# Kernel optimization log

Hardware: AMD Instinct MI355X
Metric: run time of the kernel (lower is better)

## Reference

```python
import jax, jax.numpy as jnp
import numpy as np

S, HID = 2048, 4096
H, KV, D = 32, 8, 128
EPS = 1e-6
THETA = 10000.0


def setup_inputs() -> dict:
    key = jax.random.key(0)
    k0, k1, k2 = jax.random.split(key, 3)
    return {
        "positions": jnp.arange(S, dtype=jnp.int32),
        "hidden_states": jax.random.normal(k0, (S, HID), jnp.float32),
        "w_qkv": jax.random.normal(k1, ((H + 2 * KV) * D, HID), jnp.float32) * 0.02,
        "w_o": jax.random.normal(k2, (HID, H * D), jnp.float32) * 0.02,
        "gq": jnp.ones((D,), jnp.float32),
        "gk": jnp.ones((D,), jnp.float32),
    }


def _rmsnorm(x, g):
    # per-head RMSNorm over last dim (head_dim)
    return x * jax.lax.rsqrt(jnp.mean(x * x, axis=-1, keepdims=True) + EPS) * g


def _rope(x, positions):
    # NeoX-style rotary embedding, rotary_dim == head_dim
    half = D // 2
    inv_freq = 1.0 / (THETA ** (jnp.arange(half, dtype=jnp.float32) * 2.0 / D))
    freqs = positions.astype(jnp.float32)[:, None] * inv_freq  # [S, half]
    cos = jnp.cos(freqs)[:, None, :]  # [S, 1, half]
    sin = jnp.sin(freqs)[:, None, :]
    x1, x2 = x[..., :half], x[..., half:]
    return jnp.concatenate([x1 * cos - x2 * sin, x2 * cos + x1 * sin], axis=-1)


def reference(positions, hidden_states, w_qkv, w_o, gq, gk):
    qkv = hidden_states @ w_qkv.T  # [S, (H+2KV)*D]
    q = qkv[:, : H * D].reshape(S, H, D)
    k = qkv[:, H * D : (H + KV) * D].reshape(S, KV, D)
    v = qkv[:, (H + KV) * D :].reshape(S, KV, D)

    q = _rmsnorm(q, gq)
    k = _rmsnorm(k, gk)
    q = _rope(q, positions)
    k = _rope(k, positions)

    rep = H // KV
    kf = jnp.repeat(k, rep, axis=1)  # [S, H, D]
    vf = jnp.repeat(v, rep, axis=1)

    scale = D ** -0.5
    scores = jnp.einsum("qhd,khd->hqk", q, kf) * scale  # [H, S, S]
    causal = jnp.tril(jnp.ones((S, S), dtype=bool))
    scores = jnp.where(causal[None], scores, jnp.finfo(scores.dtype).min)
    attn = jax.nn.softmax(scores, axis=-1)
    ctx = jnp.einsum("hqk,khd->qhd", attn, vf).reshape(S, H * D)
    return ctx @ w_o.T  # [S, HID]
```

## Files before the change

### kernel.cpp

```cpp
#include <hip/hip_runtime.h>
#include <hip/hip_bf16.h>

#define S_LEN 2048
#define HID   4096
#define NH    32
#define NKV   8
#define DH    128
#define NQKV  ((NH + 2*NKV) * DH)

typedef __attribute__((ext_vector_type(8))) short s16x8;
typedef __attribute__((ext_vector_type(4))) short s16x4;
typedef __attribute__((ext_vector_type(4))) float f32x4;

__device__ __forceinline__ short f2bf(float x) {
    union { __hip_bfloat16 b; short s; } u;
    u.b = __float2bfloat16(x);
    return u.s;
}
__device__ __forceinline__ float bf2f(short s) {
    union { unsigned int u; float f; } v;
    v.u = ((unsigned int)(unsigned short)s) << 16;
    return v.f;
}

__device__ __forceinline__ void gload16(const void* g, void* l) {
    __builtin_amdgcn_global_load_lds(
        (const __attribute__((address_space(1))) void*)g,
        (__attribute__((address_space(3))) void*)l,
        16, 0, 0);
}

__device__ __forceinline__ void cstore(float* p, float v) { *p = v; }
__device__ __forceinline__ void cstore(short* p, float v) { *p = f2bf(v); }

__global__ __launch_bounds__(256) void convert_hs_wqkv(
        const float* __restrict__ in1, short* __restrict__ o1, long n1,
        const float* __restrict__ in2, short* __restrict__ o2, long n2)
{
    const long total = n1 + n2;
    long i0 = ((long)blockIdx.x * blockDim.x + threadIdx.x) * 4;
    long stride = (long)gridDim.x * blockDim.x * 4;
    for (long i = i0; i < total; i += stride) {
        const float* src; short* dst; long off;
        if (i < n1) { src = in1; dst = o1; off = i; }
        else        { src = in2; dst = o2; off = i - n1; }
        float4 v = *(const float4*)(src + off);
        s16x4 o;
        o[0] = f2bf(v.x); o[1] = f2bf(v.y); o[2] = f2bf(v.z); o[3] = f2bf(v.w);
        *(s16x4*)(dst + off) = o;
    }
}

template <typename OT>
__global__ __launch_bounds__(512, 2) void gemm192(
        const short* __restrict__ A, const short* __restrict__ B,
        OT* __restrict__ C, int M, int N, int K)
{
    __shared__ char lds[114688];
    const int t = threadIdx.x;
    const int w = t >> 6, l = t & 63, g = l >> 4, q16 = l & 15;
    const int wm = w >> 2, wn = w & 3;
    const int bx = blockIdx.x, by = blockIdx.y;
    const int NT = K >> 6;

    const int r0 = t >> 3, c0 = t & 7;
    const int scA = c0 ^ (r0 & 7);
    const long KB64  = (long)K * 128;
    const long KB128 = (long)K * 256;
    const long gA00 = ((long)(by * 256 + r0) * K) * 2 + scA * 16;
    long gBoff[3];
#pragma unroll
    for (int i = 0; i < 3; ++i) {
        int row = (i * 512 + t) >> 3;
        int chunk = (t & 7) ^ (row & 7);
        gBoff[i] = ((long)(bx * 192 + row) * K) * 2 + chunk * 16;
    }
    const int dstw = w * 1024;

    auto SA = [&](int kt, int h) {
        char* d = lds + ((kt & 1) * 2 + h) * 16384 + dstw;
        const long s0 = gA00 + h * KB128 + (long)kt * 128;
        gload16((const char*)A + s0, d);
        gload16((const char*)A + s0 + KB64, d + 8192);
    };
    auto SB = [&](int kt) {
        char* d = lds + 65536 + (kt & 1) * 24576 + dstw;
        const long kb = (long)kt * 128;
#pragma unroll
        for (int i = 0; i < 3; ++i)
            gload16((const char*)B + gBoff[i] + kb, d + i * 8192);
    };

    const int arow = q16 * 128;
    const int brow = (wn * 48 + q16) * 128;
    const int sw0 = ((g) ^ (q16 & 7)) << 4;
    const int sw1 = ((4 + g) ^ (q16 & 7)) << 4;

    f32x4 acc[8][3] = {};
    s16x8 a0f[4][2], a1f[4][2], bfE[3][2], bfO[3][2];

    SB(0); SA(0, 0); SA(0, 1);
    SB(1); SA(1, 0); SA(1, 1);
    asm volatile("s_waitcnt vmcnt(7)" ::: "memory");
    __builtin_amdgcn_s_barrier();
    asm volatile("" ::: "memory");
    {
        const char* As_ = lds + wm * 16384;
        const char* Bs_ = lds + 65536;
#pragma unroll
        for (int mi = 0; mi < 4; ++mi) {
            a0f[mi][0] = *(const s16x8*)(As_ + arow + mi*2048 + sw0);
            a0f[mi][1] = *(const s16x8*)(As_ + arow + mi*2048 + sw1);
        }
#pragma unroll
        for (int ni = 0; ni < 3; ++ni) {
            bfE[ni][0] = *(const s16x8*)(Bs_ + brow + ni*2048 + sw0);
            bfE[ni][1] = *(const s16x8*)(Bs_ + brow + ni*2048 + sw1);
        }
    }

#define GBODY(KT, BCUR, BNXT, PAR) do {                                       \
    const char* As_ = lds + ((PAR)*2 + wm) * 16384;                           \
                                  \
    _Pragma("unroll")                                                         \
    for (int mi = 0; mi < 4; ++mi) {                                          \
        a1f[mi][0] = *(const s16x8*)(As_ + arow + 8192 + mi*2048 + sw0);      \
        a1f[mi][1] = *(const s16x8*)(As_ + arow + 8192 + mi*2048 + sw1);      \
    }                                                                         \
    asm volatile("s_waitcnt lgkmcnt(8)" ::: "memory");        \
    __builtin_amdgcn_sched_barrier(0);                                        \
    __builtin_amdgcn_s_setprio(1);                                            \
    _Pragma("unroll")                                                         \
    for (int mi = 0; mi < 4; ++mi)                                            \
    _Pragma("unroll")                                                         \
    for (int ni = 0; ni < 3; ++ni)                                            \
    _Pragma("unroll")                                                         \
    for (int kk = 0; kk < 2; ++kk)                                            \
        acc[mi][ni] = __builtin_amdgcn_mfma_f32_16x16x32_bf16(                \
                a0f[mi][kk], BCUR[ni][kk], acc[mi][ni], 0, 0, 0);             \
    __builtin_amdgcn_s_setprio(0);                                            \
    asm volatile("s_waitcnt lgkmcnt(0)" ::: "memory");        \
    __builtin_amdgcn_sched_barrier(0);                                        \
    __builtin_amdgcn_s_barrier();          \
    if ((KT) + 2 < NT) {                                                      \
        SB((KT) + 2); SA((KT) + 2, 0); SA((KT) + 2, 1);                       \
        asm volatile("s_waitcnt vmcnt(7)" ::: "memory");     \
    } else {                                                                  \
        asm volatile("s_waitcnt vmcnt(0)" ::: "memory");                      \
    }                                                                         \
    __builtin_amdgcn_s_barrier();               \
    asm volatile("" ::: "memory");                                            \
    if ((KT) + 1 < NT) {                    \
        const char* An_ = lds + (((PAR) ^ 1) * 2 + wm) * 16384;               \
        const char* Bn_ = lds + 65536 + ((PAR) ^ 1) * 24576;                  \
        _Pragma("unroll")                                                     \
        for (int mi = 0; mi < 4; ++mi) {                                      \
            a0f[mi][0] = *(const s16x8*)(An_ + arow + mi*2048 + sw0);         \
            a0f[mi][1] = *(const s16x8*)(An_ + arow + mi*2048 + sw1);         \
        }                                                                     \
        _Pragma("unroll")                                                     \
        for (int ni = 0; ni < 3; ++ni) {                                      \
            BNXT[ni][0] = *(const s16x8*)(Bn_ + brow + ni*2048 + sw0);        \
            BNXT[ni][1] = *(const s16x8*)(Bn_ + brow + ni*2048 + sw1);        \
        }                                                                     \
    }                                                                         \
    __builtin_amdgcn_s_setprio(1);         \
    _Pragma("unroll")                                                         \
    for (int mi = 0; mi < 4; ++mi)                                            \
    _Pragma("unroll")                                                         \
    for (int ni = 0; ni < 3; ++ni)                                            \
    _Pragma("unroll")                                                         \
    for (int kk = 0; kk < 2; ++kk)                                            \
        acc[4+mi][ni] = __builtin_amdgcn_mfma_f32_16x16x32_bf16(              \
                a1f[mi][kk], BCUR[ni][kk], acc[4+mi][ni], 0, 0, 0);           \
    __builtin_amdgcn_s_setprio(0);                                            \
} while (0)

    for (int kt = 0; kt < NT; kt += 2) {
        GBODY(kt,     bfE, bfO, 0);
        GBODY(kt + 1, bfO, bfE, 1);
    }
#undef GBODY

#pragma unroll
    for (int mf = 0; mf < 8; ++mf) {
        long row = (long)by * 256 + wm * 128 + mf * 16 + g * 4;
#pragma unroll
        for (int nf = 0; nf < 3; ++nf) {
            long col = (long)bx * 192 + wn * 48 + nf * 16 + q16;
            f32x4 v = acc[mf][nf];
#pragma unroll
            for (int r = 0; r < 4; ++r)
                cstore(&C[(row + r) * (long)N + col], v[r]);
        }
    }
}

template <typename OT>
__global__ __launch_bounds__(512, 4) void gemm_bt(
        const short* __restrict__ A, const short* __restrict__ B,
        OT* __restrict__ C, int M, int N, int K)
{
    __shared__ char lds[64 * 1024];
    const int t = threadIdx.x;
    const int w = t >> 6, l = t & 63, g = l >> 4, q16 = l & 15;
    const int wm = w >> 2, wn = w & 3;
    const long rowA = (long)blockIdx.y * 128;
    const long rowB = (long)blockIdx.x * 128;
    const int NT = K >> 6;

    long goffA[2], goffB[2];
#pragma unroll
    for (int i = 0; i < 2; ++i) {
        int li = i * 512 + t;
        int row = li >> 3;
        int chunk = (t & 7) ^ (row & 7);
        goffA[i] = ((rowA + row) * (long)K) * 2 + chunk * 16;
        goffB[i] = ((rowB + row) * (long)K) * 2 + chunk * 16;
    }
    const int ldsoff = w * 1024;

    int aoff[4][2], boff[2][2];
#pragma unroll
    for (int m = 0; m < 4; ++m)
#pragma unroll
        for (int k = 0; k < 2; ++k) {
            int row = wm * 64 + m * 16 + q16;
            int chunk = (k * 4 + g) ^ (row & 7);
            aoff[m][k] = row * 128 + chunk * 16;
        }
#pragma unroll
    for (int n = 0; n < 2; ++n)
#pragma unroll
        for (int k = 0; k < 2; ++k) {
            int row = wn * 32 + n * 16 + q16;
            int chunk = (k * 4 + g) ^ (row & 7);
            boff[n][k] = row * 128 + chunk * 16;
        }

    auto STAGE = [&](int kt, char* dA, char* dB) {
        const long kb = (long)kt * 128;
#pragma unroll
        for (int i = 0; i < 2; ++i)
            gload16((const char*)A + goffA[i] + kb, dA + i * 8192 + ldsoff);
#pragma unroll
        for (int i = 0; i < 2; ++i)
            gload16((const char*)B + goffB[i] + kb, dB + i * 8192 + ldsoff);
    };

    f32x4 acc[4][2] = {};

    STAGE(0, lds, lds + 32768);
    STAGE(1, lds + 16384, lds + 49152);

    for (int kt = 0; kt < NT; ++kt) {
        const int b = kt & 1;
        char* bA = lds + (b ? 16384 : 0);
        char* bB = lds + (b ? 49152 : 32768);
        if (kt + 1 < NT) asm volatile("s_waitcnt vmcnt(4)" ::: "memory");
        else             asm volatile("s_waitcnt vmcnt(0)" ::: "memory");
        __builtin_amdgcn_s_barrier();

        s16x8 af[4][2], bfr[2][2];
#pragma unroll
        for (int m = 0; m < 4; ++m)
#pragma unroll
            for (int k = 0; k < 2; ++k)
                af[m][k] = *(const s16x8*)(bA + aoff[m][k]);
#pragma unroll
        for (int n = 0; n < 2; ++n)
#pragma unroll
            for (int k = 0; k < 2; ++k)
                bfr[n][k] = *(const s16x8*)(bB + boff[n][k]);

        __builtin_amdgcn_s_setprio(1);
#pragma unroll
        for (int m = 0; m < 4; ++m)
#pragma unroll
            for (int n = 0; n < 2; ++n)
#pragma unroll
                for (int k = 0; k < 2; ++k)
                    acc[m][n] = __builtin_amdgcn_mfma_f32_16x16x32_bf16(
                            af[m][k], bfr[n][k], acc[m][n], 0, 0, 0);
        __builtin_amdgcn_s_setprio(0);
        __builtin_amdgcn_s_barrier();

        if (kt + 2 < NT) STAGE(kt + 2, bA, bB);
    }

#pragma unroll
    for (int m = 0; m < 4; ++m) {
        long row = rowA + wm * 64 + m * 16 + g * 4;
#pragma unroll
        for (int n = 0; n < 2; ++n) {
            long col = rowB + wn * 32 + n * 16 + q16;
            f32x4 v = acc[m][n];
#pragma unroll
            for (int r = 0; r < 4; ++r)
                cstore(&C[(row + r) * (long)N + col], v[r]);
        }
    }
}

__global__ __launch_bounds__(256) void post_gemm1_fused(
        const float* __restrict__ wo, short* __restrict__ wob,
        const short* __restrict__ qkvb, const int* __restrict__ pos,
        const float* __restrict__ gq, const float* __restrict__ gk,
        short* __restrict__ qo, short* __restrict__ ko,
        short* __restrict__ vt)
{
    const int bid = blockIdx.x;

    if (bid < 2048) {
        const long n = (long)HID * (NH * DH);
        long i0 = ((long)bid * 256 + threadIdx.x) * 4;
        long stride = 2048L * 256 * 4;
        for (long i = i0; i < n; i += stride) {
            float4 v = *(const float4*)(wo + i);
            s16x4 o;
            o[0] = f2bf(v.x); o[1] = f2bf(v.y); o[2] = f2bf(v.z); o[3] = f2bf(v.w);
            *(s16x4*)(wob + i) = o;
        }
        return;
    }

    if (bid < 12288) {
        const int idx = bid - 2048;
        const int s = idx / 5;
        const int slot = (idx % 5) * 8 + (threadIdx.x >> 5);
        const int p = threadIdx.x & 31, d = p * 4;

        s16x4 xv = *(const s16x4*)(qkvb + (long)s * NQKV + slot * DH + d);
        float x[4];
#pragma unroll
        for (int r = 0; r < 4; ++r) x[r] = bf2f(xv[r]);

        float ss = x[0]*x[0] + x[1]*x[1] + x[2]*x[2] + x[3]*x[3];
#pragma unroll
        for (int o = 1; o < 32; o <<= 1) ss += __shfl_xor(ss, o);
        float rms = rsqrtf(ss * (1.0f / DH) + 1e-6f);

        const bool isq = slot < NH;
        const float* gp = isq ? gq : gk;
        float y[4];
#pragma unroll
        for (int r = 0; r < 4; ++r) y[r] = x[r] * rms * gp[d + r];

        float y2[4];
#pragma unroll
        for (int r = 0; r < 4; ++r) y2[r] = __shfl_xor(y[r], 16);

        const float po = (float)pos[s];
        const int jbase = d & 63;
        s16x4 ov;
#pragma unroll
        for (int r = 0; r < 4; ++r) {
            float invf = exp2f(-(float)(jbase + r) * (13.287712379549449f / 64.0f));
            float ang = po * invf;
            float c = cosf(ang), sn = sinf(ang);
            float outv = (d < 64) ? (y[r] * c - y2[r] * sn)
                                  : (y[r] * c + y2[r] * sn);
            ov[r] = f2bf(outv);
        }
        if (isq) *(s16x4*)(qo + ((long)s * NH + slot) * DH + d) = ov;
        else     *(s16x4*)(ko + ((long)s * NKV + (slot - NH)) * DH + d) = ov;
        return;
    }

    __shared__ short tile[64][72];
    const int idx2 = bid - 12288;
    const int sb = idx2 & 31, db = (idx2 >> 5) & 1, h = idx2 >> 6;
    const int t = threadIdx.x;
#pragma unroll
    for (int i = 0; i < 2; ++i) {
        int c = i * 256 + t;
        int row = c >> 3, dc = (c & 7) * 8;
        const short* src = qkvb + (long)(sb*64 + row) * NQKV
                           + (NH + NKV + h) * DH + db*64 + dc;
        s16x8 x = *(const s16x8*)src;
#pragma unroll
        for (int jj = 0; jj < 8; ++jj) tile[row][dc + jj] = x[jj];
    }
    __syncthreads();
#pragma unroll
    for (int i = 0; i < 2; ++i) {
        int c = i * 256 + t;
        int dr = c >> 3, sc = (c & 7) * 8;
        s16x8 y;
#pragma unroll
        for (int jj = 0; jj < 8; ++jj) y[jj] = tile[sc + jj][dr];
        short* dst = vt + (long)(h*DH + db*64 + dr) * S_LEN + sb*64 + sc;
        *(s16x8*)dst = y;
    }
}

__device__ __forceinline__ void stage_kv(const char* kgB, const char* vgB,
                                         int kt, int t, char* kd, char* vd)
{
    const int w = t >> 6;
#pragma unroll
    for (int ci = 0; ci < 4; ++ci) {
        int c = ci * 256 + t;
        int row = c >> 4, col16 = c & 15;
        const char* gk = kgB + (long)(kt*64 + row) * (NKV*DH*2)
                         + ((col16*16) ^ ((row & 7) << 4));
        gload16(gk, kd + ci*4096 + w*1024);
        int rowv = c >> 3, scol8 = c & 7;
        const char* gv = vgB + (long)rowv * (S_LEN*2) + kt*128
                         + ((scol8*16) ^ ((rowv & 7) << 4));
        gload16(gv, vd + ci*4096 + w*1024);
    }
}

__global__ __launch_bounds__(256, 2) void attn_kernel(
        const short* __restrict__ qg, const short* __restrict__ kg,
        const short* __restrict__ vtg, short* __restrict__ ctx)
{
    const int bx = blockIdx.x;
    const int h  = bx & 31;
    const int slot = bx >> 5;
    const int qb = (slot < 8) ? slot : 23 - slot;
    const int kvh = h >> 2;
    const int t = threadIdx.x, w = t >> 6, l = t & 63, g = l >> 4, q16 = l & 15;

    __shared__ char Kl[2][16384];
    __shared__ char Vl[2][16384];
    __shared__ short Pl[4][32 * 64];

    const float scale = 0.08838834764831845f;
    const char* kgB = (const char*)kg + (long)kvh * DH * 2;
    const char* vgB = (const char*)vtg + (long)kvh * DH * (long)S_LEN * 2;

    const int nt = 2 * qb + 2;
    int qrow[2];
    qrow[0] = qb*128 + w*32 + q16;
    qrow[1] = qrow[0] + 16;

    s16x8 qf[2][4];
#pragma unroll
    for (int s = 0; s < 2; ++s) {
        const short* qptr = qg + ((long)qrow[s] * NH + h) * DH;
#pragma unroll
        for (int dk = 0; dk < 4; ++dk)
            qf[s][dk] = *(const s16x8*)(qptr + dk*32 + g*8);
    }

    f32x4 oacc[2][8] = {};
    float m_run[2] = {-1e30f, -1e30f}, l_run[2] = {0.f, 0.f};

    stage_kv(kgB, vgB, 0, t, Kl[0], Vl[0]);
    __syncthreads();

    for (int kt = 0; kt < nt; ++kt) {
        const int b = kt & 1;
        if (kt + 1 < nt)
            stage_kv(kgB, vgB, kt + 1, t, Kl[b ^ 1], Vl[b ^ 1]);
        const char* kb = Kl[b];
        const char* vbb = Vl[b];

        f32x4 sacc[2][4] = {};
        __builtin_amdgcn_s_setprio(1);
#pragma unroll
        for (int m = 0; m < 4; ++m) {
            int kvr = m*16 + q16;
            s16x8 af[4];
#pragma unroll
            for (int dk = 0; dk < 4; ++dk) {
                int byte = (kvr*256 + (dk*32 + g*8)*2) ^ ((kvr & 7) << 4);
                af[dk] = *(const s16x8*)(kb + byte);
            }
#pragma unroll
            for (int s = 0; s < 2; ++s)
#pragma unroll
                for (int dk = 0; dk < 4; ++dk)
                    sacc[s][m] = __builtin_amdgcn_mfma_f32_16x16x32_bf16(
                            af[dk], qf[s][dk], sacc[s][m], 0,0,0);
        }
        __builtin_amdgcn_s_setprio(0);

        const bool diag = (kt >= 2*qb);
        float mx[2];
#pragma unroll
        for (int s = 0; s < 2; ++s) {
            mx[s] = -1e30f;
#pragma unroll
            for (int m = 0; m < 4; ++m)
#pragma unroll
                for (int r = 0; r < 4; ++r) {
                    float x = sacc[s][m][r] * scale;
                    if (diag) {
                        int kv = kt*64 + m*16 + g*4 + r;
                        if (kv > qrow[s]) x = -1e30f;
                    }
                    sacc[s][m][r] = x;
                    mx[s] = fmaxf(mx[s], x);
                }
            mx[s] = fmaxf(mx[s], __shfl_xor(mx[s], 16));
            mx[s] = fmaxf(mx[s], __shfl_xor(mx[s], 32));
        }
        if (__any((mx[0] > m_run[0] + 8.f) || (mx[1] > m_run[1] + 8.f))) {
#pragma unroll
            for (int s = 0; s < 2; ++s) {
                float m_new = fmaxf(m_run[s], mx[s]);
                float corr = __expf(m_run[s] - m_new);
                l_run[s] *= corr;
                m_run[s] = m_new;
                float rf[4];
#pragma unroll
                for (int r = 0; r < 4; ++r)
                    rf[r] = __shfl(corr, (g << 4) | (g*4 + r));
#pragma unroll
                for (int nf = 0; nf < 8; ++nf)
#pragma unroll
                    for (int r = 0; r < 4; ++r) oacc[s][nf][r] *= rf[r];
            }
        }
#pragma unroll
        for (int s = 0; s < 2; ++s) {
            float psum = 0.f;
#pragma unroll
            for (int m = 0; m < 4; ++m) {
                s16x4 pk;
#pragma unroll
                for (int r = 0; r < 4; ++r) {
                    float e = __expf(sacc[s][m][r] - m_run[s]);
                    psum += e;
                    pk[r] = f2bf(e);
                }
                int byte = ((s*16 + q16)*128 + (m*16 + g*4)*2) ^ ((q16 & 7) << 4);
                *(s16x4*)((char*)&Pl[w][0] + byte) = pk;
            }
            psum += __shfl_xor(psum, 16);
            psum += __shfl_xor(psum, 32);
            l_run[s] += psum;
        }

        __builtin_amdgcn_s_setprio(1);
#pragma unroll
        for (int ks = 0; ks < 2; ++ks) {
            s16x8 pa[2];
#pragma unroll
            for (int s = 0; s < 2; ++s) {
                int pbyte = ((s*16 + q16)*128 + (ks*32 + g*8)*2) ^ ((q16 & 7) << 4);
                pa[s] = *(const s16x8*)((const char*)&Pl[w][0] + pbyte);
            }
#pragma unroll
            for (int nf = 0; nf < 8; ++nf) {
                int drow = nf*16 + q16;
                int vbyte = (drow*128 + (ks*32 + g*8)*2) ^ ((drow & 7) << 4);
                s16x8 vbf = *(const s16x8*)(vbb + vbyte);
#pragma unroll
                for (int s = 0; s < 2; ++s)
                    oacc[s][nf] = __builtin_amdgcn_mfma_f32_16x16x32_bf16(
                            pa[s], vbf, oacc[s][nf], 0,0,0);
            }
        }
        __builtin_amdgcn_s_setprio(0);
        __syncthreads();
    }

#pragma unroll
    for (int s = 0; s < 2; ++s) {
        float lr[4];
#pragma unroll
        for (int r = 0; r < 4; ++r)
            lr[r] = __shfl(l_run[s], (g << 4) | (g*4 + r));
#pragma unroll
        for (int nf = 0; nf < 8; ++nf)
#pragma unroll
            for (int r = 0; r < 4; ++r) {
                int row = qb*128 + w*32 + s*16 + g*4 + r;
                int col = h*DH + nf*16 + q16;
                float val = oacc[s][nf][r] / lr[r];
                ctx[(long)row * (NH*DH) + col] = f2bf(val);
            }
    }
}

extern "C" void kernel_launch(void* const* d_in, const int* in_sizes, int n_in,
                              void* d_out, int out_size, void* d_ws, size_t ws_size,
                              hipStream_t stream)
{
    const int*   positions = (const int*)  d_in[0];
    const float* hs        = (const float*)d_in[1];
    const float* wqkv      = (const float*)d_in[2];
    const float* wo        = (const float*)d_in[3];
    const float* gq        = (const float*)d_in[4];
    const float* gk        = (const float*)d_in[5];
    float* out = (float*)d_out;
    char* ws = (char*)d_ws;

    const size_t MB = 1ull << 20;
    short* hsb   = (short*)(ws);
    short* ctxb  = (short*)(ws);
    short* wqkvb = (short*)(ws + 16*MB);
    short* wob   = (short*)(ws + 16*MB);
    short* vtbuf = (short*)(ws + 48*MB);
    short* qkvb  = (short*)(ws + 67*MB);
    short* qbuf  = (short*)(ws + 91*MB);
    short* kbuf  = (short*)(ws + 107*MB);

    (void)in_sizes; (void)n_in; (void)out_size; (void)ws_size;

    convert_hs_wqkv<<<2048, 256, 0, stream>>>(
            hs, hsb, (long)S_LEN * HID,
            wqkv, wqkvb, (long)NQKV * HID);
    gemm192<short><<<dim3(NQKV/192, S_LEN/256), 512, 0, stream>>>(
            hsb, wqkvb, qkvb, S_LEN, NQKV, HID);
    post_gemm1_fused<<<12800, 256, 0, stream>>>(
            wo, wob, qkvb, positions, gq, gk, qbuf, kbuf, vtbuf);
    attn_kernel<<<dim3(512), 256, 0, stream>>>(qbuf, kbuf, vtbuf, ctxb);
    gemm_bt<float><<<dim3(HID/128, S_LEN/128), 512, 0, stream>>>(
            ctxb, wob, out, S_LEN, HID, HID);
}
```

Baseline: 302.0 us.

## Retile QKV GEMM to 128x192 blocks with 4 waves and 2x2 warp layout

The QKV projection GEMM moves from 512-thread 256x192 blocks to 256-thread 128x192 blocks. Each wave now computes a 64x96 tile instead of 128x48, and LDS drops from 112KB to 80KB. The pipeline keeps A fragments double-buffered across iterations and loads B per step, waiting on vmcnt(0) before issuing the next stage. The grid doubles in the M direction, which raises block count and occupancy but lowers per-block reuse and weakens load/compute overlap.

```diff
diff --git a/kernel.cpp b/kernel.cpp
--- a/kernel.cpp
+++ b/kernel.cpp
@@ -52,82 +52,77 @@
 }
 
 template <typename OT>
-__global__ __launch_bounds__(512, 2) void gemm192(
+__global__ __launch_bounds__(256, 2) void gemm192(
         const short* __restrict__ A, const short* __restrict__ B,
         OT* __restrict__ C, int M, int N, int K)
 {
-    __shared__ char lds[114688];
+    __shared__ char lds[81920];
     const int t = threadIdx.x;
     const int w = t >> 6, l = t & 63, g = l >> 4, q16 = l & 15;
-    const int wm = w >> 2, wn = w & 3;
+    const int wm = w >> 1, wn = w & 1;
     const int bx = blockIdx.x, by = blockIdx.y;
     const int NT = K >> 6;
 
-    const int r0 = t >> 3, c0 = t & 7;
-    const int scA = c0 ^ (r0 & 7);
-    const long KB64  = (long)K * 128;
-    const long KB128 = (long)K * 256;
-    const long gA00 = ((long)(by * 256 + r0) * K) * 2 + scA * 16;
-    long gBoff[3];
-#pragma unroll
-    for (int i = 0; i < 3; ++i) {
-        int row = (i * 512 + t) >> 3;
-        int chunk = (t & 7) ^ (row & 7);
-        gBoff[i] = ((long)(bx * 192 + row) * K) * 2 + chunk * 16;
-    }
+    const int srow = t >> 3;
+    const int schunk = (t & 7) ^ (srow & 7);
+    unsigned goffA[4], goffB[6];
+#pragma unroll
+    for (int i = 0; i < 4; ++i)
+        goffA[i] = (unsigned)(((by * 128 + i * 32 + srow) * K) * 2 + schunk * 16);
+#pragma unroll
+    for (int i = 0; i < 6; ++i)
+        goffB[i] = (unsigned)(((bx * 192 + i * 32 + srow) * K) * 2 + schunk * 16);
     const int dstw = w * 1024;
 
-    auto SA = [&](int kt, int h) {
-        char* d = lds + ((kt & 1) * 2 + h) * 16384 + dstw;
-        const long s0 = gA00 + h * KB128 + (long)kt * 128;
-        gload16((const char*)A + s0, d);
-        gload16((const char*)A + s0 + KB64, d + 8192);
+    auto STAGE = [&](int kt) {
+        const int par = kt & 1;
+        char* dA = lds + par * 16384 + dstw;
+        char* dB = lds + 32768 + par * 24576 + dstw;
+        const unsigned kb = (unsigned)kt * 128;
+#pragma unroll
+        for (int i = 0; i < 4; ++i)
+            gload16((const char*)A + (goffA[i] + kb), dA + i * 4096);
+#pragma unroll
+        for (int i = 0; i < 6; ++i)
+            gload16((const char*)B + (goffB[i] + kb), dB + i * 4096);
     };
-    auto SB = [&](int kt) {
-        char* d = lds + 65536 + (kt & 1) * 24576 + dstw;
-        const long kb = (long)kt * 128;
-#pragma unroll
-        for (int i = 0; i < 3; ++i)
-            gload16((const char*)B + gBoff[i] + kb, d + i * 8192);
-    };
-
-    const int arow = q16 * 128;
-    const int brow = (wn * 48 + q16) * 128;
+
+    int aoff[4], boff[6];
+#pragma unroll
+    for (int mi = 0; mi < 4; ++mi) aoff[mi] = (wm * 64 + mi * 16 + q16) * 128;
+#pragma unroll
+    for (int ni = 0; ni < 6; ++ni) boff[ni] = (wn * 96 + ni * 16 + q16) * 128;
     const int sw0 = ((g) ^ (q16 & 7)) << 4;
     const int sw1 = ((4 + g) ^ (q16 & 7)) << 4;
 
-    f32x4 acc[8][3] = {};
-    s16x8 a0f[4][2], a1f[4][2], bfE[3][2], bfO[3][2];
-
-    SB(0); SA(0, 0); SA(0, 1);
-    SB(1); SA(1, 0); SA(1, 1);
-    asm volatile("s_waitcnt vmcnt(7)" ::: "memory");
+    f32x4 acc[4][6] = {};
+    s16x8 aE[4][2], aO[4][2], b0f[3][2], b1f[3][2];
+
+    STAGE(0); STAGE(1);
+    asm volatile("s_waitcnt vmcnt(10)" ::: "memory");
     __builtin_amdgcn_s_barrier();
-    asm volatile("" ::: "memory");
     {
-        const char* As_ = lds + wm * 16384;
-        const char* Bs_ = lds + 65536;
+        const char* A0 = lds;
 #pragma unroll
         for (int mi = 0; mi < 4; ++mi) {
-            a0f[mi][0] = *(const s16x8*)(As_ + arow + mi*2048 + sw0);
-            a0f[mi][1] = *(const s16x8*)(As_ + arow + mi*2048 + sw1);
-        }
-#pragma unroll
-        for (int ni = 0; ni < 3; ++ni) {
-            bfE[ni][0] = *(const s16x8*)(Bs_ + brow + ni*2048 + sw0);
-            bfE[ni][1] = *(const s16x8*)(Bs_ + brow + ni*2048 + sw1);
-        }
-    }
-
-#define GBODY(KT, BCUR, BNXT, PAR) do {                                       \
-    const char* As_ = lds + ((PAR)*2 + wm) * 16384;                           \
-                                  \
-    _Pragma("unroll")                                                         \
-    for (int mi = 0; mi < 4; ++mi) {                                          \
-        a1f[mi][0] = *(const s16x8*)(As_ + arow + 8192 + mi*2048 + sw0);      \
-        a1f[mi][1] = *(const s16x8*)(As_ + arow + 8192 + mi*2048 + sw1);      \
+            aE[mi][0] = *(const s16x8*)(A0 + aoff[mi] + sw0);
+            aE[mi][1] = *(const s16x8*)(A0 + aoff[mi] + sw1);
+        }
+    }
+
+#define GB(KT, AC, AN, PAR) do {                                              \
+    const char* Bs_ = lds + 32768 + (PAR) * 24576;                            \
+    _Pragma("unroll")                                                         \
+    for (int ni = 0; ni < 3; ++ni) {                                          \
+        b0f[ni][0] = *(const s16x8*)(Bs_ + boff[ni] + sw0);                   \
+        b0f[ni][1] = *(const s16x8*)(Bs_ + boff[ni] + sw1);                   \
     }                                                                         \
-    asm volatile("s_waitcnt lgkmcnt(8)" ::: "memory");        \
+    _Pragma("unroll")                                                         \
+    for (int ni = 0; ni < 3; ++ni) {                                          \
+        b1f[ni][0] = *(const s16x8*)(Bs_ + boff[3 + ni] + sw0);               \
+        b1f[ni][1] = *(const s16x8*)(Bs_ + boff[3 + ni] + sw1);               \
+    }                                                                         \
+    asm volatile("s_waitcnt lgkmcnt(6)" ::: "memory");       \
     __builtin_amdgcn_sched_barrier(0);                                        \
     __builtin_amdgcn_s_setprio(1);                                            \
     _Pragma("unroll")                                                         \
@@ -137,58 +132,46 @@
     _Pragma("unroll")                                                         \
     for (int kk = 0; kk < 2; ++kk)                                            \
         acc[mi][ni] = __builtin_amdgcn_mfma_f32_16x16x32_bf16(                \
-                a0f[mi][kk], BCUR[ni][kk], acc[mi][ni], 0, 0, 0);             \
+                AC[mi][kk], b0f[ni][kk], acc[mi][ni], 0, 0, 0);               \
     __builtin_amdgcn_s_setprio(0);                                            \
-    asm volatile("s_waitcnt lgkmcnt(0)" ::: "memory");        \
+    asm volatile("s_waitcnt lgkmcnt(0)" ::: "memory");           \
     __builtin_amdgcn_sched_barrier(0);                                        \
-    __builtin_amdgcn_s_barrier();          \
-    if ((KT) + 2 < NT) {                                                      \
-        SB((KT) + 2); SA((KT) + 2, 0); SA((KT) + 2, 1);                       \
-        asm volatile("s_waitcnt vmcnt(7)" ::: "memory");     \
-    } else {                                                                  \
-        asm volatile("s_waitcnt vmcnt(0)" ::: "memory");                      \
-    }                                                                         \
-    __builtin_amdgcn_s_barrier();               \
-    asm volatile("" ::: "memory");                                            \
-    if ((KT) + 1 < NT) {                    \
-        const char* An_ = lds + (((PAR) ^ 1) * 2 + wm) * 16384;               \
-        const char* Bn_ = lds + 65536 + ((PAR) ^ 1) * 24576;                  \
+    asm volatile("s_waitcnt vmcnt(0)" ::: "memory");        \
+    __builtin_amdgcn_s_barrier();       \
+    if ((KT) + 2 < NT) STAGE((KT) + 2);                                       \
+    if ((KT) + 1 < NT) {                      \
+        const char* An_ = lds + (((PAR) ^ 1) * 16384);                        \
         _Pragma("unroll")                                                     \
         for (int mi = 0; mi < 4; ++mi) {                                      \
-            a0f[mi][0] = *(const s16x8*)(An_ + arow + mi*2048 + sw0);         \
-            a0f[mi][1] = *(const s16x8*)(An_ + arow + mi*2048 + sw1);         \
-        }                                                                     \
-        _Pragma("unroll")                                                     \
-        for (int ni = 0; ni < 3; ++ni) {                                      \
-            BNXT[ni][0] = *(const s16x8*)(Bn_ + brow + ni*2048 + sw0);        \
-            BNXT[ni][1] = *(const s16x8*)(Bn_ + brow + ni*2048 + sw1);        \
+            AN[mi][0] = *(const s16x8*)(An_ + aoff[mi] + sw0);                \
+            AN[mi][1] = *(const s16x8*)(An_ + aoff[mi] + sw1);                \
         }                                                                     \
     }                                                                         \
-    __builtin_amdgcn_s_setprio(1);         \
+    __builtin_amdgcn_s_setprio(1);                                            \
     _Pragma("unroll")                                                         \
     for (int mi = 0; mi < 4; ++mi)                                            \
     _Pragma("unroll")                                                         \
     for (int ni = 0; ni < 3; ++ni)                                            \
     _Pragma("unroll")                                                         \
     for (int kk = 0; kk < 2; ++kk)                                            \
-        acc[4+mi][ni] = __builtin_amdgcn_mfma_f32_16x16x32_bf16(              \
-                a1f[mi][kk], BCUR[ni][kk], acc[4+mi][ni], 0, 0, 0);           \
+        acc[mi][3 + ni] = __builtin_amdgcn_mfma_f32_16x16x32_bf16(            \
+                AC[mi][kk], b1f[ni][kk], acc[mi][3 + ni], 0, 0, 0);           \
     __builtin_amdgcn_s_setprio(0);                                            \
 } while (0)
 
     for (int kt = 0; kt < NT; kt += 2) {
-        GBODY(kt,     bfE, bfO, 0);
-        GBODY(kt + 1, bfO, bfE, 1);
-    }
-#undef GBODY
-
-#pragma unroll
-    for (int mf = 0; mf < 8; ++mf) {
-        long row = (long)by * 256 + wm * 128 + mf * 16 + g * 4;
-#pragma unroll
-        for (int nf = 0; nf < 3; ++nf) {
-            long col = (long)bx * 192 + wn * 48 + nf * 16 + q16;
-            f32x4 v = acc[mf][nf];
+        GB(kt,     aE, aO, 0);
+        GB(kt + 1, aO, aE, 1);
+    }
+#undef GB
+
+#pragma unroll
+    for (int mi = 0; mi < 4; ++mi) {
+        long row = (long)by * 128 + wm * 64 + mi * 16 + g * 4;
+#pragma unroll
+        for (int ni = 0; ni < 6; ++ni) {
+            long col = (long)bx * 192 + wn * 96 + ni * 16 + q16;
+            f32x4 v = acc[mi][ni];
 #pragma unroll
             for (int r = 0; r < 4; ++r)
                 cstore(&C[(row + r) * (long)N + col], v[r]);
@@ -605,7 +588,7 @@
     convert_hs_wqkv<<<2048, 256, 0, stream>>>(
             hs, hsb, (long)S_LEN * HID,
             wqkv, wqkvb, (long)NQKV * HID);
-    gemm192<short><<<dim3(NQKV/192, S_LEN/256), 512, 0, stream>>>(
+    gemm192<short><<<dim3(NQKV/192, S_LEN/128), 256, 0, stream>>>(
             hsb, wqkvb, qkvb, S_LEN, NQKV, HID);
     post_gemm1_fused<<<12800, 256, 0, stream>>>(
             wo, wob, qkvb, positions, gq, gk, qbuf, kbuf, vtbuf);
```

Result: no change. 303.5 us (+0.5%).
